# Performance work log

Hardware: AMD Instinct MI355X
Metric: run time of the kernel (lower is better)

Reference implementation:

```python
import jax, jax.numpy as jnp
import numpy as np

RAD2DEG = 180.0 / 3.14159  # module uses 3.14159, not pi

def _conv2d(x, w):
    # x: (N,1,H,W), w: (O,1,3,3), SAME padding, stride 1
    return jax.lax.conv_general_dilated(
        x, w, window_strides=(1, 1), padding='SAME',
        dimension_numbers=('NCHW', 'OIHW', 'NCHW'))

def _make_filters():
    sobel = np.array([[1, 0, -1], [2, 0, -2], [1, 0, -1]], dtype=np.float32)
    f0   = [[0,0,0],[0,1,-1],[0,0,0]]
    f45  = [[0,0,0],[0,1,0],[0,0,-1]]
    f90  = [[0,0,0],[0,1,0],[0,-1,0]]
    f135 = [[0,0,0],[0,1,0],[-1,0,0]]
    f180 = [[0,0,0],[-1,1,0],[0,0,0]]
    f225 = [[-1,0,0],[0,1,0],[0,0,0]]
    f270 = [[0,-1,0],[0,1,0],[0,0,0]]
    f315 = [[0,0,-1],[0,1,0],[0,0,0]]
    dirs = np.stack([f0,f45,f90,f135,f180,f225,f270,f315]).astype(np.float32)
    return sobel, dirs

def setup_inputs() -> dict:
    key = jax.random.key(0)
    H, W = 2160, 3840
    img = jax.random.uniform(key, (1, 3, H, W), dtype=jnp.float32)
    sobel, dirs = _make_filters()
    sobel_h = jnp.asarray(sobel)[None, None]          # (1,1,3,3)
    sobel_v = jnp.asarray(sobel.T)[None, None]        # (1,1,3,3)
    dir_w = jnp.asarray(dirs)[:, None]                # (8,1,3,3)
    return {"img": img, "sobel_h": sobel_h, "sobel_v": sobel_v, "dir_w": dir_w}

def reference(img, sobel_h, sobel_v, dir_w):
    # grayscale: mean of the 3 channels
    gray = (img[:, 0:1] + img[:, 1:2] + img[:, 2:3]) / 3.0        # (1,1,H,W)
    grad_x = _conv2d(gray, sobel_h)
    grad_y = _conv2d(gray, sobel_v)
    grad_mag = jnp.sqrt(grad_x ** 2 + grad_y ** 2)                # (1,1,H,W)
    # orientation in degrees, snapped to multiples of 45 (round-half-even, like torch.round)
    ori = jnp.round((jnp.arctan2(grad_y, grad_x) * RAD2DEG + 180.0) / 45.0)
    idx_pos = jnp.mod(ori, 8.0).astype(jnp.int32)                 # (1,1,H,W)
    idx_neg = jnp.mod(ori + 4.0, 8.0).astype(jnp.int32)
    all_filtered = _conv2d(grad_mag, dir_w)                       # (1,8,H,W)
    # per-pixel channel select (the flattened gather in the original)
    pos = jnp.take_along_axis(all_filtered, idx_pos, axis=1)      # (1,1,H,W)
    neg = jnp.take_along_axis(all_filtered, idx_neg, axis=1)
    is_max = jnp.minimum(pos, neg) > 0.0
    # in-place aliasing in the original: thin_edges/early_threshold alias grad_mag,
    # so the final binary map is: is_max AND (grad_mag >= 0.2)
    th = jnp.where(is_max & (grad_mag >= 0.2), 1.0, 0.0).astype(jnp.float32)
    return th
```

## Files before the change

### kernel.cpp

```cpp
#include <hip/hip_runtime.h>
#include <math.h>

#define IMG_W 3840
#define IMG_H 2160
#define OUTW  60
#define R     12
#define GROWS (R + 4)

#define DXPACK 0x901A
#define DYPACK 0x1A9

#define T1_SLOPE 0.41421317376456f
#define T2_SLOPE 2.41420676743300f
#define SECT_EPS 3.0e-5f

__device__ __noinline__ int slow_sector(float sx, float sy) {
#pragma clang fp contract(off)
    const float RADF = (float)(180.0 / 3.14159);
    float t = atan2f(sy, sx);
    float wv = ((t * RADF) + 180.0f) / 45.0f;
    float ori = rintf(wv);
    float fr = fabsf(wv - ori);
    if (fr > 0.4995f) {
        double td = atan2((double)sy, (double)sx);
        float t2 = (float)td;
        wv = ((t2 * RADF) + 180.0f) / 45.0f;
        ori = rintf(wv);
    }
    return ((int)ori) & 7;
}


#define LOADROW(kk, cj)                                                        \
    {                                                                          \
        const int y_  = Y0 - 2 + (kk);                                         \
        const int yc_ = min(max(y_, 0), IMG_H - 1);                            \
        const int o_  = yc_ * IMG_W + xc;                                      \
        c0[(cj)] = img[o_];                                                    \
        c1[(cj)] = im1[o_];                                                    \
        c2[(cj)] = im2[o_];                                                    \
    }

#define GRAY(kk, cj, j3)                                                       \
    {                                                                          \
        const int  y_   = Y0 - 2 + (kk);                                       \
        const bool yok_ = (unsigned)y_ < (unsigned)IMG_H;                      \
        float t_  = ((c0[(cj)] + c1[(cj)]) + c2[(cj)]) / 3.0f;                 \
        float gv_ = (xok && yok_) ? t_ : 0.0f;                                 \
        g[(j3)]  = gv_;                                                        \
        gl[(j3)] = __shfl_up(gv_, 1);                                          \
        gr[(j3)] = __shfl_down(gv_, 1);                                        \
    }

#define MAGROW(kk, j3, DONMS)                                                  \
    {                                                                          \
        const int i0_ = ((j3) + 2) & 3, i1_ = ((j3) + 3) & 3, i2_ = (j3);      \
        float a00 = gl[i0_], a01 = g[i0_], a02 = gr[i0_];                      \
        float a10 = gl[i1_],               a12 = gr[i1_];                      \
        float a20 = gl[i2_], a21 = g[i2_], a22 = gr[i2_];                      \
        float sx = a00;                                \
        sx = sx - a02;                                                         \
        sx = sx + 2.0f * a10;                                                  \
        sx = sx - 2.0f * a12;                                                  \
        sx = sx + a20;                                                         \
        sx = sx - a22;                                                         \
        float sy = a00;                                                        \
        sy = sy + 2.0f * a01;                                                  \
        sy = sy + a02;                                                         \
        sy = sy - a20;                                                         \
        sy = sy - 2.0f * a21;                                                  \
        sy = sy - a22;                                                         \
        float magv = sqrtf(sx * sx + sy * sy);                                 \
        float ax = fabsf(sx), ay = fabsf(sy);                                  \
        float d1 = fmaf(-T1_SLOPE, ax, ay);                                    \
        float d2 = fmaf(-T2_SLOPE, ax, ay);                                    \
        float sA = ax + ay;                                                    \
        int dxo, dyo;                                                          \
        if (__builtin_expect(fabsf(d1) < SECT_EPS * sA ||                      \
                             fabsf(d2) < SECT_EPS * sA, 0)) {                  \
            int idx = slow_sector(sx, sy);                                     \
            dxo = ((DXPACK >> (2 * idx)) & 3) - 1;                             \
            dyo = ((DYPACK >> (2 * idx)) & 3) - 1;                             \
        } else {                                                               \
            dxo = (d2 > 0.0f) ? 0 : ((sx > 0.0f) ? -1 : 1);                    \
            dyo = (d1 < 0.0f) ? 0 : ((sy > 0.0f) ? -1 : 1);                    \
        }                                                                      \
        const bool vok_ = xmok && ((unsigned)(Y0 - 3 + (kk)) < (unsigned)IMG_H); \
        float mag_  = vok_ ? magv : 0.0f;                                      \
        int   offv_ = vok_ ? (dyo * 64 + dxo) : 0;                             \
        B[(((j3) + 2) & 3) * 64 + lane] = mag_;    \
        if (DONMS) {                                                           \
            \
            const int rp_  = (((j3) + 1) & 3) * 64;                            \
            const int ipp_ = (rp_ + lane + off_p) & 255;                       \
            const int ipn_ = (rp_ + lane - off_p) & 255;                       \
            float mp_ = B[ipp_];                                               \
            float mn_ = B[ipn_];                                               \
            float res_ = (fminf(mc_p - mp_, mc_p - mn_) > 0.0f &&              \
                          mc_p >= 0.2f) ? 1.0f : 0.0f;                         \
            if (xoutok)                                                        \
                out[(size_t)(Y0 + (kk) - 4) * IMG_W + x] = res_;               \
        }                                                                      \
        mc_p  = mag_;                                                          \
        off_p = offv_;                                                         \
    }

__global__ __launch_bounds__(256, 4) void canny_like_kernel(const float* __restrict__ img,
                                                            float* __restrict__ out) {
#pragma clang fp contract(off)
    __shared__ float lds_m[4][4][64];

    const int lane = threadIdx.x;
    const int w    = threadIdx.y;
    const int X0   = (blockIdx.x * 4 + w) * OUTW;
    const int Y0   = blockIdx.y * R;
    const int x    = X0 - 2 + lane;
    const bool xok    = (unsigned)x < (unsigned)IMG_W;
    const int  xc     = min(max(x, 0), IMG_W - 1);
    const bool xmok   = (lane >= 1) && (lane <= 62) && xok;
    const bool xoutok = (lane >= 2) && (lane <= 61);

    const float* im1 = img + (size_t)IMG_W * IMG_H;
    const float* im2 = img + 2 * (size_t)IMG_W * IMG_H;

    float* const B = &lds_m[w][0][0];

    float c0[8], c1[8], c2[8];
    float g[4], gl[4], gr[4];
    float mc_p  = 0.0f;
    int   off_p = 0;

    LOADROW(0, 0)  LOADROW(1, 1)  LOADROW(2, 2)  LOADROW(3, 3)
    LOADROW(4, 4)  LOADROW(5, 5)  LOADROW(6, 6)  LOADROW(7, 7)

    GRAY(0, 0, 0)  LOADROW( 8, 0)
    GRAY(1, 1, 1)  LOADROW( 9, 1)
    GRAY(2, 2, 2)  LOADROW(10, 2)  MAGROW(2, 2, 0)
    GRAY(3, 3, 3)  LOADROW(11, 3)  MAGROW(3, 3, 0)
    GRAY(4, 4, 0)  LOADROW(12, 4)  MAGROW(4, 0, 1)
    GRAY(5, 5, 1)  LOADROW(13, 5)  MAGROW(5, 1, 1)
    GRAY(6, 6, 2)  LOADROW(14, 6)  MAGROW(6, 2, 1)
    GRAY(7, 7, 3)  LOADROW(15, 7)  MAGROW(7, 3, 1)

    GRAY( 8, 0, 0)  MAGROW( 8, 0, 1)
    GRAY( 9, 1, 1)  MAGROW( 9, 1, 1)
    GRAY(10, 2, 2)  MAGROW(10, 2, 1)
    GRAY(11, 3, 3)  MAGROW(11, 3, 1)
    GRAY(12, 4, 0)  MAGROW(12, 0, 1)
    GRAY(13, 5, 1)  MAGROW(13, 1, 1)
    GRAY(14, 6, 2)  MAGROW(14, 2, 1)
    GRAY(15, 7, 3)  MAGROW(15, 3, 1)
}

extern "C" void kernel_launch(void* const* d_in, const int* in_sizes, int n_in,
                              void* d_out, int out_size, void* d_ws, size_t ws_size,
                              hipStream_t stream) {
    const float* img = (const float*)d_in[0];
    float* out = (float*)d_out;
    dim3 grid(64 / 4, IMG_H / R);
    dim3 block(64, 4);
    canny_like_kernel<<<grid, block, 0, stream>>>(img, out);
}
```

Before: 163.3 us.

## Batch Sobel rows in groups of four and hoist slow-sector fixup out of per-row branch

Processes magnitude/orientation for four rows at a time into an 8-row LDS ring, then runs the rare slow atan2 sector fixup once per group under a single wave-uniform branch before doing NMS for the group. The aim is to cut per-row divergent branches around the noinline slow_sector call and give the compiler more independent work to interleave. The trade-off is more live registers (8-deep gray ring plus four rows of temporaries) and doubled LDS per wave, which could hurt occupancy.

```diff
diff --git a/kernel.cpp b/kernel.cpp
--- a/kernel.cpp
+++ b/kernel.cpp
@@ -41,20 +41,20 @@
         c2[(cj)] = im2[o_];                                                    \
     }
 
-#define GRAY(kk, cj, j3)                                                       \
+#define GRAY8(kk, cj, j7)                                                      \
     {                                                                          \
         const int  y_   = Y0 - 2 + (kk);                                       \
         const bool yok_ = (unsigned)y_ < (unsigned)IMG_H;                      \
         float t_  = ((c0[(cj)] + c1[(cj)]) + c2[(cj)]) / 3.0f;                 \
         float gv_ = (xok && yok_) ? t_ : 0.0f;                                 \
-        g[(j3)]  = gv_;                                                        \
-        gl[(j3)] = __shfl_up(gv_, 1);                                          \
-        gr[(j3)] = __shfl_down(gv_, 1);                                        \
-    }
-
-#define MAGROW(kk, j3, DONMS)                                                  \
-    {                                                                          \
-        const int i0_ = ((j3) + 2) & 3, i1_ = ((j3) + 3) & 3, i2_ = (j3);      \
+        g[(j7)]  = gv_;                                                        \
+        gl[(j7)] = __shfl_up(gv_, 1);                                          \
+        gr[(j7)] = __shfl_down(gv_, 1);                                       \
+    }
+
+#define SOBEL(kk, MG, OF, SX, SY, CC)                                          \
+    {                                                                          \
+        const int i0_ = ((kk) + 6) & 7, i1_ = ((kk) + 7) & 7, i2_ = (kk) & 7;  \
         float a00 = gl[i0_], a01 = g[i0_], a02 = gr[i0_];                      \
         float a10 = gl[i1_],               a12 = gr[i1_];                      \
         float a20 = gl[i2_], a21 = g[i2_], a22 = gr[i2_];                      \
@@ -75,40 +75,42 @@
         float d1 = fmaf(-T1_SLOPE, ax, ay);                                    \
         float d2 = fmaf(-T2_SLOPE, ax, ay);                                    \
         float sA = ax + ay;                                                    \
-        int dxo, dyo;                                                          \
-        if (__builtin_expect(fabsf(d1) < SECT_EPS * sA ||                      \
-                             fabsf(d2) < SECT_EPS * sA, 0)) {                  \
-            int idx = slow_sector(sx, sy);                                     \
-            dxo = ((DXPACK >> (2 * idx)) & 3) - 1;                             \
-            dyo = ((DYPACK >> (2 * idx)) & 3) - 1;                             \
-        } else {                                                               \
-            dxo = (d2 > 0.0f) ? 0 : ((sx > 0.0f) ? -1 : 1);                    \
-            dyo = (d1 < 0.0f) ? 0 : ((sy > 0.0f) ? -1 : 1);                    \
-        }                                                                      \
+        (SX) = sx; (SY) = sy;                                                  \
+        (CC) = (fabsf(d1) < SECT_EPS * sA) || (fabsf(d2) < SECT_EPS * sA);     \
+        int dxo = (d2 > 0.0f) ? 0 : ((sx > 0.0f) ? -1 : 1);                    \
+        int dyo = (d1 < 0.0f) ? 0 : ((sy > 0.0f) ? -1 : 1);                    \
         const bool vok_ = xmok && ((unsigned)(Y0 - 3 + (kk)) < (unsigned)IMG_H); \
-        float mag_  = vok_ ? magv : 0.0f;                                      \
-        int   offv_ = vok_ ? (dyo * 64 + dxo) : 0;                             \
-        B[(((j3) + 2) & 3) * 64 + lane] = mag_;    \
-        if (DONMS) {                                                           \
-            \
-            const int rp_  = (((j3) + 1) & 3) * 64;                            \
-            const int ipp_ = (rp_ + lane + off_p) & 255;                       \
-            const int ipn_ = (rp_ + lane - off_p) & 255;                       \
-            float mp_ = B[ipp_];                                               \
-            float mn_ = B[ipn_];                                               \
-            float res_ = (fminf(mc_p - mp_, mc_p - mn_) > 0.0f &&              \
-                          mc_p >= 0.2f) ? 1.0f : 0.0f;                         \
-            if (xoutok)                                                        \
-                out[(size_t)(Y0 + (kk) - 4) * IMG_W + x] = res_;               \
-        }                                                                      \
-        mc_p  = mag_;                                                          \
-        off_p = offv_;                                                         \
+        (MG) = vok_ ? magv : 0.0f;                                             \
+        (OF) = vok_ ? (dyo * 64 + dxo) : 0;                                    \
+        B[((kk) & 7) * 64 + lane] = (MG);                  \
+    }
+
+#define FIXROW(kk, OF, SX, SY, CC)                                             \
+    if (CC) {                                                                  \
+        int idx_ = slow_sector((SX), (SY));                                    \
+        int dxo_ = ((DXPACK >> (2 * idx_)) & 3) - 1;                           \
+        int dyo_ = ((DYPACK >> (2 * idx_)) & 3) - 1;                           \
+        const bool vok_ = xmok && ((unsigned)(Y0 - 3 + (kk)) < (unsigned)IMG_H); \
+        (OF) = vok_ ? (dyo_ * 64 + dxo_) : 0;                                  \
+    }
+
+#define NMSROW(M, MC, OFC)                                                     \
+    {                                                                          \
+        const int rp_  = ((M) & 7) * 64;                                       \
+        const int ipp_ = (rp_ + lane + (OFC)) & 511;                           \
+        const int ipn_ = (rp_ + lane - (OFC)) & 511;                           \
+        float mp_ = B[ipp_];                                                   \
+        float mn_ = B[ipn_];                                                   \
+        float res_ = (fminf((MC) - mp_, (MC) - mn_) > 0.0f &&                  \
+                      (MC) >= 0.2f) ? 1.0f : 0.0f;                             \
+        if (xoutok)                                                            \
+            out[(size_t)(Y0 + (M) - 3) * IMG_W + x] = res_;                    \
     }
 
 __global__ __launch_bounds__(256, 4) void canny_like_kernel(const float* __restrict__ img,
                                                             float* __restrict__ out) {
 #pragma clang fp contract(off)
-    __shared__ float lds_m[4][4][64];
+    __shared__ float lds_m[4][8][64];
 
     const int lane = threadIdx.x;
     const int w    = threadIdx.y;
@@ -126,30 +128,88 @@
     float* const B = &lds_m[w][0][0];
 
     float c0[8], c1[8], c2[8];
-    float g[4], gl[4], gr[4];
-    float mc_p  = 0.0f;
-    int   off_p = 0;
+    float g[8], gl[8], gr[8];
 
     LOADROW(0, 0)  LOADROW(1, 1)  LOADROW(2, 2)  LOADROW(3, 3)
     LOADROW(4, 4)  LOADROW(5, 5)  LOADROW(6, 6)  LOADROW(7, 7)
 
-    GRAY(0, 0, 0)  LOADROW( 8, 0)
-    GRAY(1, 1, 1)  LOADROW( 9, 1)
-    GRAY(2, 2, 2)  LOADROW(10, 2)  MAGROW(2, 2, 0)
-    GRAY(3, 3, 3)  LOADROW(11, 3)  MAGROW(3, 3, 0)
-    GRAY(4, 4, 0)  LOADROW(12, 4)  MAGROW(4, 0, 1)
-    GRAY(5, 5, 1)  LOADROW(13, 5)  MAGROW(5, 1, 1)
-    GRAY(6, 6, 2)  LOADROW(14, 6)  MAGROW(6, 2, 1)
-    GRAY(7, 7, 3)  LOADROW(15, 7)  MAGROW(7, 3, 1)
-
-    GRAY( 8, 0, 0)  MAGROW( 8, 0, 1)
-    GRAY( 9, 1, 1)  MAGROW( 9, 1, 1)
-    GRAY(10, 2, 2)  MAGROW(10, 2, 1)
-    GRAY(11, 3, 3)  MAGROW(11, 3, 1)
-    GRAY(12, 4, 0)  MAGROW(12, 0, 1)
-    GRAY(13, 5, 1)  MAGROW(13, 1, 1)
-    GRAY(14, 6, 2)  MAGROW(14, 2, 1)
-    GRAY(15, 7, 3)  MAGROW(15, 3, 1)
+    GRAY8(0, 0, 0)  LOADROW(8, 0)
+    GRAY8(1, 1, 1)  LOADROW(9, 1)
+
+    float mA, mB, mC, mD;
+    int   oA, oB, oC, oD;
+    float sxA, syA, sxB, syB, sxC, syC, sxD, syD;
+    int   cA, cB, cC, cD;
+    float mc_p;  int off_p;
+
+    GRAY8(2, 2, 2)  LOADROW(10, 2)
+    GRAY8(3, 3, 3)  LOADROW(11, 3)
+    GRAY8(4, 4, 4)  LOADROW(12, 4)
+    GRAY8(5, 5, 5)  LOADROW(13, 5)
+    SOBEL(2, mA, oA, sxA, syA, cA)
+    SOBEL(3, mB, oB, sxB, syB, cB)
+    SOBEL(4, mC, oC, sxC, syC, cC)
+    SOBEL(5, mD, oD, sxD, syD, cD)
+    if (__builtin_expect(cA | cB | cC | cD, 0)) {
+        FIXROW(2, oA, sxA, syA, cA)
+        FIXROW(3, oB, sxB, syB, cB)
+        FIXROW(4, oC, sxC, syC, cC)
+        FIXROW(5, oD, sxD, syD, cD)
+    }
+    NMSROW(3, mB, oB)
+    NMSROW(4, mC, oC)
+    mc_p = mD;  off_p = oD;
+
+    GRAY8(6, 6, 6)  LOADROW(14, 6)
+    GRAY8(7, 7, 7)  LOADROW(15, 7)
+    GRAY8(8, 0, 0)
+    GRAY8(9, 1, 1)
+    SOBEL(6, mA, oA, sxA, syA, cA)
+    SOBEL(7, mB, oB, sxB, syB, cB)
+    SOBEL(8, mC, oC, sxC, syC, cC)
+    SOBEL(9, mD, oD, sxD, syD, cD)
+    if (__builtin_expect(cA | cB | cC | cD, 0)) {
+        FIXROW(6, oA, sxA, syA, cA)
+        FIXROW(7, oB, sxB, syB, cB)
+        FIXROW(8, oC, sxC, syC, cC)
+        FIXROW(9, oD, sxD, syD, cD)
+    }
+    NMSROW(5, mc_p, off_p)
+    NMSROW(6, mA, oA)
+    NMSROW(7, mB, oB)
+    NMSROW(8, mC, oC)
+    mc_p = mD;  off_p = oD;
+
+    GRAY8(10, 2, 2)
+    GRAY8(11, 3, 3)
+    GRAY8(12, 4, 4)
+    GRAY8(13, 5, 5)
+    SOBEL(10, mA, oA, sxA, syA, cA)
+    SOBEL(11, mB, oB, sxB, syB, cB)
+    SOBEL(12, mC, oC, sxC, syC, cC)
+    SOBEL(13, mD, oD, sxD, syD, cD)
+    if (__builtin_expect(cA | cB | cC | cD, 0)) {
+        FIXROW(10, oA, sxA, syA, cA)
+        FIXROW(11, oB, sxB, syB, cB)
+        FIXROW(12, oC, sxC, syC, cC)
+        FIXROW(13, oD, sxD, syD, cD)
+    }
+    NMSROW(9,  mc_p, off_p)
+    NMSROW(10, mA, oA)
+    NMSROW(11, mB, oB)
+    NMSROW(12, mC, oC)
+    mc_p = mD;  off_p = oD;
+
+    GRAY8(14, 6, 6)
+    GRAY8(15, 7, 7)
+    SOBEL(14, mA, oA, sxA, syA, cA)
+    SOBEL(15, mB, oB, sxB, syB, cB)
+    if (__builtin_expect(cA | cB, 0)) {
+        FIXROW(14, oA, sxA, syA, cA)
+        FIXROW(15, oB, sxB, syB, cB)
+    }
+    NMSROW(13, mc_p, off_p)
+    NMSROW(14, mA, oA)
 }
 
 extern "C" void kernel_launch(void* const* d_in, const int* in_sizes, int n_in,
```

Result: no change. 164.3 us (+0.6%).
